# Kernel tuning notes

Hardware: AMD Instinct MI355X
Metric: run time of the kernel (lower is better)

The kernel has to match this reference:

```python
import jax, jax.numpy as jnp
import numpy as np

B, N, C = 4, 2048, 768
H, HD = 12, 64
RANK, ALPHA = 8, 16.0
SCALING = ALPHA / RANK
SCALE = HD ** -0.5


def setup_inputs() -> dict:
    key = jax.random.key(0)
    ks = jax.random.split(key, 10)
    return {
        "x": jax.random.normal(ks[0], (B, N, C), jnp.float32),
        "qkv_weight": jax.random.normal(ks[1], (3 * C, C), jnp.float32) * 0.02,
        "q_bias": jax.random.normal(ks[2], (C,), jnp.float32) * 0.02,
        "v_bias": jax.random.normal(ks[3], (C,), jnp.float32) * 0.02,
        "lora_A_qkv": jax.random.normal(ks[4], (RANK, C), jnp.float32) * 0.02,
        "lora_B_qkv": jax.random.normal(ks[5], (3 * C, RANK), jnp.float32) * 0.02,
        "proj_weight": jax.random.normal(ks[6], (C, C), jnp.float32) * 0.02,
        "proj_bias": jax.random.normal(ks[7], (C,), jnp.float32) * 0.02,
        "lora_A_proj": jax.random.normal(ks[8], (RANK, C), jnp.float32) * 0.02,
        "lora_B_proj": jax.random.normal(ks[9], (C, RANK), jnp.float32) * 0.02,
    }


def reference(x, qkv_weight, q_bias, v_bias, lora_A_qkv, lora_B_qkv,
              proj_weight, proj_bias, lora_A_proj, lora_B_proj):
    # qkv bias = [q_bias, zeros, v_bias]
    qkv_bias = jnp.concatenate([q_bias, jnp.zeros_like(v_bias), v_bias])
    qkv = jnp.einsum('bnc,oc->bno', x, qkv_weight) + qkv_bias  # [B,N,3C]
    # LoRA on qkv: (x @ A^T @ B^T) * scaling
    qkv = qkv + jnp.einsum('bnr,or->bno', jnp.einsum('bnc,rc->bnr', x, lora_A_qkv), lora_B_qkv) * SCALING
    qkv = qkv.reshape(B, N, 3, H, HD).transpose(2, 0, 3, 1, 4)  # [3,B,H,N,HD]
    q, k, v = qkv[0], qkv[1], qkv[2]
    attn = jnp.einsum('bhnd,bhmd->bhnm', q * SCALE, k)  # [B,H,N,N]
    attn = jax.nn.softmax(attn, axis=-1)
    out = jnp.einsum('bhnm,bhmd->bhnd', attn, v)
    out = out.transpose(0, 2, 1, 3).reshape(B, N, C)
    out = jnp.einsum('bnc,oc->bno', out, proj_weight) + proj_bias
    # NOTE: module applies proj LoRA to the OUTPUT of proj (faithful quirk)
    out = out + jnp.einsum('bnr,or->bno', jnp.einsum('bnc,rc->bnr', out, lora_A_proj), lora_B_proj) * SCALING
    return out
```

## Files before the change

### kernel.cpp

```cpp
#include <hip/hip_runtime.h>
#include <cstdint>
#include <cstddef>

typedef __bf16 bf16;
typedef __bf16 bf16x2_t __attribute__((ext_vector_type(2)));
typedef __bf16 bf16x4_t __attribute__((ext_vector_type(4)));
typedef __bf16 bf16x8_t __attribute__((ext_vector_type(8)));
typedef float f32x4_t __attribute__((ext_vector_type(4)));
typedef unsigned int u32;
typedef u32 u32x2_t __attribute__((ext_vector_type(2)));

#define DEV __device__ __forceinline__

static constexpr int CD  = 768;
static constexpr int C3  = 2304;
static constexpr int SEQ = 2048;
static constexpr int NB  = 4;
static constexpr int NH  = 12;
static constexpr int HDM = 64;
static constexpr int BHN = NB * NH;
static constexpr float QSCALE = 0.125f * 1.44269504088896340736f;
static constexpr float DEFER_THR = 4.0f;

DEV void async16(const void* g, void* l) {
  __builtin_amdgcn_global_load_lds(
      (const __attribute__((address_space(1))) void*)g,
      (__attribute__((address_space(3))) void*)l, 16, 0, 0);
}

DEV int swz(int r) { return (r ^ (r >> 2)) & 3; }

DEV u32 pack_bf16(float lo, float hi) {
  bf16x2_t v;
  v[0] = (bf16)lo;
  v[1] = (bf16)hi;
  return __builtin_bit_cast(u32, v);
}

DEV float max3f(float a, float b, float c) { return fmaxf(fmaxf(a, b), c); }

__global__ void k_prep_a(const float* __restrict__ x, bf16* __restrict__ xb,
                         const float* __restrict__ W, const float* __restrict__ Aq,
                         const float* __restrict__ Bq, bf16* __restrict__ We,
                         const float* __restrict__ Ap, const float* __restrict__ Wp,
                         float* __restrict__ T,
                         const float* __restrict__ bp, const float* __restrict__ Bp,
                         float* __restrict__ be) {
  __shared__ float smem[4][64];
  const int bid = blockIdx.x, tid = threadIdx.x;
  if (bid < 6912) {
    int idx = bid * 256 + tid;
    int o = idx / CD, c = idx % CD;
    float s = 0.f;
#pragma unroll
    for (int r = 0; r < 8; ++r) s += Bq[o * 8 + r] * Aq[r * CD + c];
    We[idx] = (bf16)(W[idx] + 2.0f * s);
  } else if (bid < 7008) {
    const int lb = bid - 6912;
    const int r = lb / 12, cp0 = (lb % 12) * 64;
    const int kl = tid >> 6, cpl = tid & 63;
    float s = 0.f;
    const int c0 = kl * 192;
    for (int c = c0; c < c0 + 192; ++c)
      s += Ap[r * CD + c] * Wp[(size_t)c * CD + cp0 + cpl];
    smem[kl][cpl] = s;
    __syncthreads();
    if (tid < 64)
      T[r * CD + cp0 + tid] = (smem[0][tid] + smem[1][tid]) +
                              (smem[2][tid] + smem[3][tid]);
  } else if (bid == 7008) {
    float* tl = &smem[0][0];
    const int r = tid >> 5, cl = tid & 31;
    float part = 0.f;
    for (int c = cl; c < CD; c += 32) part += Ap[r * CD + c] * bp[c];
#pragma unroll
    for (int d = 1; d < 32; d <<= 1) part += __shfl_xor(part, d);
    if (cl == 0) tl[r] = part;
    __syncthreads();
    for (int o = tid; o < CD; o += 256) {
      float s = 0.f;
#pragma unroll
      for (int rr = 0; rr < 8; ++rr) s += Bp[o * 8 + rr] * tl[rr];
      be[o] = bp[o] + 2.0f * s;
    }
  } else {
    const int n4 = (int)((size_t)NB * SEQ * CD / 4);
    int i = (bid - 7009) * 256 + tid;
    const int stride = 2048 * 256;
    for (; i < n4; i += stride) {
      float4 v = reinterpret_cast<const float4*>(x)[i];
      bf16x4_t b;
      b[0] = (bf16)v.x; b[1] = (bf16)v.y; b[2] = (bf16)v.z; b[3] = (bf16)v.w;
      reinterpret_cast<bf16x4_t*>(xb)[i] = b;
    }
  }
}

__global__ void k_prep_projw(const float* __restrict__ Wp, const float* __restrict__ Bp,
                             const float* __restrict__ T, bf16* __restrict__ We) {
  int idx = blockIdx.x * 256 + threadIdx.x;
  int o = idx / CD, cp = idx % CD;
  float s = 0.f;
#pragma unroll
  for (int r = 0; r < 8; ++r) s += Bp[o * 8 + r] * T[r * CD + cp];
  We[idx] = (bf16)(Wp[idx] + 2.0f * s);
}

__global__ __launch_bounds__(512) void k_gemm0(
    const bf16* __restrict__ Ag, const bf16* __restrict__ Bg,
    const float* __restrict__ qb, const float* __restrict__ vb,
    bf16* __restrict__ Qo, bf16* __restrict__ Ko, bf16* __restrict__ Vt) {
  __shared__ bf16 lds[2][(256 + 128) * 32];
  const int tid = threadIdx.x;
  const int w = tid >> 6, lane = tid & 63;
  const int lr = lane & 15, lg = lane >> 4;
  const int L = blockIdx.x;
  const int idx = L >> 3;
  const int m0 = ((L & 7) * 4 + idx / 18) * 256;
  const int n0 = (idx % 18) * 128;
  const int wm = w >> 1, wn = w & 1;

  const int r0 = tid >> 2, gp0 = tid & 3;
  const bf16* gA0 = Ag + (size_t)(m0 + r0) * CD + (gp0 ^ swz(r0)) * 8;
  const bf16* gA1 = Ag + (size_t)(m0 + 128 + r0) * CD + (gp0 ^ swz(r0)) * 8;
  const bf16* gB0 = Bg + (size_t)(n0 + r0) * CD + (gp0 ^ swz(r0)) * 8;

  f32x4_t acc[4][4] = {};

  auto stage = [&](int buf, int kof) {
    char* base = (char*)&lds[buf][0];
    async16(gA0 + kof, base + w * 1024);
    async16(gA1 + kof, base + 8192 + w * 1024);
    async16(gB0 + kof, base + 16384 + w * 1024);
  };

  stage(0, 0);
  int cur = 0;
  const int NK = CD / 32;
  for (int kt = 0; kt < NK; ++kt) {
    __syncthreads();
    if (kt + 1 < NK) stage(cur ^ 1, (kt + 1) * 32);
    const char* ba = (const char*)&lds[cur][0];
    const char* bb = ba + 16384;
    bf16x8_t af[4], bfr[4];
#pragma unroll
    for (int mi = 0; mi < 4; ++mi) {
      int rr = wm * 64 + mi * 16 + lr;
      af[mi] = *(const bf16x8_t*)(ba + rr * 64 + ((lg ^ swz(rr)) * 16));
    }
#pragma unroll
    for (int ni = 0; ni < 4; ++ni) {
      int rr = wn * 64 + ni * 16 + lr;
      bfr[ni] = *(const bf16x8_t*)(bb + rr * 64 + ((lg ^ swz(rr)) * 16));
    }
#pragma unroll
    for (int mi = 0; mi < 4; ++mi)
#pragma unroll
      for (int ni = 0; ni < 4; ++ni)
        acc[mi][ni] = __builtin_amdgcn_mfma_f32_16x16x32_bf16(bfr[ni], af[mi], acc[mi][ni], 0, 0, 0);
    cur ^= 1;
  }

  const int t = n0 / CD;
  if (t != 2) {
#pragma unroll
    for (int mi = 0; mi < 4; ++mi) {
      const int m = m0 + wm * 64 + mi * 16 + lr;
      const int b = m >> 11, nn = m & 2047;
#pragma unroll
      for (int ni = 0; ni < 4; ++ni) {
        const int nb = n0 + wn * 64 + ni * 16 + lg * 4;
        const int rem = nb - t * CD;
        const int h = rem >> 6, hd = rem & 63;
        const size_t oa = ((size_t)((b * NH + h) * SEQ + nn)) * HDM + hd;
        bf16x4_t o4;
        if (t == 0) {
          const float4 bias = *(const float4*)(qb + rem);
          o4[0] = (bf16)((acc[mi][ni][0] + bias.x) * QSCALE);
          o4[1] = (bf16)((acc[mi][ni][1] + bias.y) * QSCALE);
          o4[2] = (bf16)((acc[mi][ni][2] + bias.z) * QSCALE);
          o4[3] = (bf16)((acc[mi][ni][3] + bias.w) * QSCALE);
          *(bf16x4_t*)(Qo + oa) = o4;
        } else {
#pragma unroll
          for (int j = 0; j < 4; ++j) o4[j] = (bf16)acc[mi][ni][j];
          *(bf16x4_t*)(Ko + oa) = o4;
        }
      }
    }
  } else {
    bf16* tl = (bf16*)&lds[0][0];
    const int h0 = (n0 - 2 * CD) >> 6;
    const int bq = m0 >> 11;
    const int mb = m0 & 2047;
    const int r2 = tid >> 2, c2 = (tid & 3) * 32;
#pragma unroll
    for (int half = 0; half < 2; ++half) {
      __syncthreads();
      if ((wm >> 1) == half) {
#pragma unroll
        for (int mi = 0; mi < 4; ++mi) {
          const int ml = (wm & 1) * 64 + mi * 16 + lr;
#pragma unroll
          for (int ni = 0; ni < 4; ++ni) {
            const int hd = ni * 16 + lg * 4;
            const int rem = (n0 - 2 * CD) + wn * 64 + hd;
            const float4 bias = *(const float4*)(vb + rem);
            bf16* row = tl + (wn * 64 + hd) * 136 + ml;
            row[0 * 136] = (bf16)(acc[mi][ni][0] + bias.x);
            row[1 * 136] = (bf16)(acc[mi][ni][1] + bias.y);
            row[2 * 136] = (bf16)(acc[mi][ni][2] + bias.z);
            row[3 * 136] = (bf16)(acc[mi][ni][3] + bias.w);
          }
        }
      }
      __syncthreads();
      bf16* dstv = Vt + ((size_t)((bq * NH + h0 + (r2 >> 6)) * HDM) + (r2 & 63)) * SEQ
                      + mb + half * 128 + c2;
      const bf16* srcv = tl + r2 * 136 + c2;
#pragma unroll
      for (int k2 = 0; k2 < 4; ++k2)
        *(bf16x8_t*)(dstv + k2 * 8) = *(const bf16x8_t*)(srcv + k2 * 8);
    }
  }
}

__global__ __launch_bounds__(256) void k_gemm1(
    const bf16* __restrict__ Ag, const bf16* __restrict__ Bg,
    const float* __restrict__ beff, float* __restrict__ Fo) {
  __shared__ bf16 lds[2][2][128 * 32];
  const int tid = threadIdx.x;
  const int w = tid >> 6, lane = tid & 63;
  const int lr = lane & 15, lg = lane >> 4;
  const int L = blockIdx.x;
  const int idx = L >> 3;
  const int m0 = ((L & 7) * 8 + idx / 6) * 128;
  const int n0 = (idx % 6) * 128;
  const int wm = w >> 1, wn = w & 1;

  const int r0 = tid >> 2, gp0 = tid & 3;
  const int r1 = 64 + r0;
  const bf16* gA0 = Ag + (size_t)(m0 + r0) * CD + (gp0 ^ swz(r0)) * 8;
  const bf16* gA1 = Ag + (size_t)(m0 + r1) * CD + (gp0 ^ swz(r1)) * 8;
  const bf16* gB0 = Bg + (size_t)(n0 + r0) * CD + (gp0 ^ swz(r0)) * 8;
  const bf16* gB1 = Bg + (size_t)(n0 + r1) * CD + (gp0 ^ swz(r1)) * 8;
  const int dd0 = w * 1024, dd1 = 4096 + w * 1024;

  f32x4_t acc[4][4] = {};

  auto stage = [&](int buf, int kof) {
    char* ba = (char*)&lds[buf][0][0];
    char* bb = (char*)&lds[buf][1][0];
    async16(gA0 + kof, ba + dd0);
    async16(gA1 + kof, ba + dd1);
    async16(gB0 + kof, bb + dd0);
    async16(gB1 + kof, bb + dd1);
  };

  stage(0, 0);
  int cur = 0;
  const int NK = CD / 32;
  for (int kt = 0; kt < NK; ++kt) {
    __syncthreads();
    if (kt + 1 < NK) stage(cur ^ 1, (kt + 1) * 32);
    const char* ba = (const char*)&lds[cur][0][0];
    const char* bb = (const char*)&lds[cur][1][0];
    bf16x8_t af[4], bfr[4];
#pragma unroll
    for (int mi = 0; mi < 4; ++mi) {
      int rr = wm * 64 + mi * 16 + lr;
      af[mi] = *(const bf16x8_t*)(ba + rr * 64 + ((lg ^ swz(rr)) * 16));
    }
#pragma unroll
    for (int ni = 0; ni < 4; ++ni) {
      int rr = wn * 64 + ni * 16 + lr;
      bfr[ni] = *(const bf16x8_t*)(bb + rr * 64 + ((lg ^ swz(rr)) * 16));
    }
#pragma unroll
    for (int mi = 0; mi < 4; ++mi)
#pragma unroll
      for (int ni = 0; ni < 4; ++ni)
        acc[mi][ni] = __builtin_amdgcn_mfma_f32_16x16x32_bf16(bfr[ni], af[mi], acc[mi][ni], 0, 0, 0);
    cur ^= 1;
  }

#pragma unroll
  for (int mi = 0; mi < 4; ++mi) {
    const int m = m0 + wm * 64 + mi * 16 + lr;
#pragma unroll
    for (int ni = 0; ni < 4; ++ni) {
      const int nb = n0 + wn * 64 + ni * 16 + lg * 4;
      const float4 be4 = *(const float4*)(beff + nb);
      float4 o;
      o.x = acc[mi][ni][0] + be4.x;
      o.y = acc[mi][ni][1] + be4.y;
      o.z = acc[mi][ni][2] + be4.z;
      o.w = acc[mi][ni][3] + be4.w;
      *(float4*)(Fo + (size_t)m * CD + nb) = o;
    }
  }
}

__global__ __launch_bounds__(256, 3) void k_attn(const bf16* __restrict__ Q,
                                                 const bf16* __restrict__ Kg,
                                                 const bf16* __restrict__ Vt,
                                                 bf16* __restrict__ Ao) {
  __shared__ bf16 Kl[2][64 * 64];
  __shared__ bf16 Vl[2][64 * 64];
  __shared__ bf16 P[4][32 * 72];
  const int tid = threadIdx.x;
  const int w = tid >> 6, lane = tid & 63;
  const int lq = lane & 15, lg = lane >> 4;
  const int L = blockIdx.x;
  const int qb = (L >> 3) & 15;
  const int bh = (L & 7) * 6 + (L >> 7);
  const int b = bh / NH, h = bh % NH;
  const int qrow0 = qb * 128 + w * 32;

  const bf16* Qp = Q + ((size_t)bh * SEQ + qrow0) * HDM;
  const bf16* Kp = Kg + (size_t)bh * SEQ * HDM;
  const bf16* Vp = Vt + (size_t)bh * HDM * SEQ;

  const int sr = tid >> 3, scs = tid & 7;
  const int sr2 = sr + 32;
  bf16* kb0 = &Kl[0][w * 512]; bf16* kb1 = &Kl[1][w * 512];
  bf16* vb0 = &Vl[0][w * 512]; bf16* vb1 = &Vl[1][w * 512];

  auto stageKV = [&](int buf, int kb) {
    bf16* kd = buf ? kb1 : kb0;
    bf16* vd = buf ? vb1 : vb0;
    async16(Kp + (size_t)(kb + sr) * HDM + ((scs ^ (sr & 7)) * 8), kd);
    async16(Kp + (size_t)(kb + sr2) * HDM + ((scs ^ (sr2 & 7)) * 8), kd + 2048);
    async16(Vp + (size_t)sr * SEQ + kb + ((scs ^ (sr & 7)) * 8), vd);
    async16(Vp + (size_t)sr2 * SEQ + kb + ((scs ^ (sr2 & 7)) * 8), vd + 2048);
  };

  bf16x8_t qf[2][2];
#pragma unroll
  for (int qh = 0; qh < 2; ++qh)
#pragma unroll
    for (int s = 0; s < 2; ++s)
      qf[qh][s] = *(const bf16x8_t*)(Qp + (size_t)(lq + 16 * qh) * HDM + s * 32 + lg * 8);

  bf16x8_t ones;
#pragma unroll
  for (int j = 0; j < 8; ++j) ones[j] = (bf16)1.0f;

  f32x4_t oacc[2][2][4] = {};
  float mrun[2][2] = {{-1e30f, -1e30f}, {-1e30f, -1e30f}};
  float lsum[2][2] = {{0.f, 0.f}, {0.f, 0.f}};
  bf16* Pl = &P[w][0];
  const int sw = lq & 7;

  auto body = [&](const int curbuf, const int kb) {
    __syncthreads();
    if (kb + 64 < SEQ) stageKV(curbuf ^ 1, kb + 64);
    const bf16* Kc = &Kl[curbuf][0];
    const bf16* Vc = &Vl[curbuf][0];

    f32x4_t st[2][2][2];
#pragma unroll
    for (int c = 0; c < 2; ++c)
#pragma unroll
      for (int nt = 0; nt < 2; ++nt) {
        const int row = c * 32 + nt * 16 + lq;
        bf16x8_t k0 = *(const bf16x8_t*)(Kc + row * 64 + ((lg ^ sw) * 8));
        bf16x8_t k1 = *(const bf16x8_t*)(Kc + row * 64 + (((4 + lg) ^ sw) * 8));
#pragma unroll
        for (int qh = 0; qh < 2; ++qh) {
          f32x4_t z = {0.f, 0.f, 0.f, 0.f};
          z = __builtin_amdgcn_mfma_f32_16x16x32_bf16(k0, qf[qh][0], z, 0, 0, 0);
          st[c][nt][qh] = __builtin_amdgcn_mfma_f32_16x16x32_bf16(k1, qf[qh][1], z, 0, 0, 0);
        }
      }

#pragma unroll
    for (int c = 0; c < 2; ++c)
#pragma unroll
      for (int qh = 0; qh < 2; ++qh) {
        float m = max3f(st[c][0][qh][0], st[c][0][qh][1], st[c][0][qh][2]);
        float m2 = max3f(st[c][0][qh][3], st[c][1][qh][0], st[c][1][qh][1]);
        m = max3f(m, m2, st[c][1][qh][2]);
        m = fmaxf(m, st[c][1][qh][3]);
        m = fmaxf(m, __shfl_xor(m, 16));
        m = fmaxf(m, __shfl_xor(m, 32));
        if (__any(m > mrun[c][qh] + DEFER_THR)) {
          const float mnew = fmaxf(mrun[c][qh], m);
          const float corr = __builtin_amdgcn_exp2f(mrun[c][qh] - mnew);
          mrun[c][qh] = mnew;
          lsum[c][qh] *= corr;
#pragma unroll
          for (int dt = 0; dt < 4; ++dt)
#pragma unroll
            for (int j = 0; j < 4; ++j) oacc[c][qh][dt][j] *= corr;
        }
#pragma unroll
        for (int nt = 0; nt < 2; ++nt)
#pragma unroll
          for (int j = 0; j < 4; ++j)
            st[c][nt][qh][j] = __builtin_amdgcn_exp2f(st[c][nt][qh][j] - mrun[c][qh]);

#pragma unroll
        for (int nt = 0; nt < 2; ++nt) {
          u32x2_t pw = {pack_bf16(st[c][nt][qh][0], st[c][nt][qh][1]),
                        pack_bf16(st[c][nt][qh][2], st[c][nt][qh][3])};
          *(u32x2_t*)(Pl + (lq + 16 * qh) * 72 + c * 32 + nt * 16 + lg * 4) = pw;
        }
      }

#pragma unroll
    for (int c = 0; c < 2; ++c) {
      bf16x8_t pf[2];
#pragma unroll
      for (int qh = 0; qh < 2; ++qh) {
        pf[qh] = *(const bf16x8_t*)(Pl + (lq + 16 * qh) * 72 + c * 32 + lg * 8);
        const f32x4_t zz = {0.f, 0.f, 0.f, 0.f};
        f32x4_t srow = __builtin_amdgcn_mfma_f32_16x16x32_bf16(ones, pf[qh], zz, 0, 0, 0);
        lsum[c][qh] += srow[0];
      }
#pragma unroll
      for (int dt = 0; dt < 4; ++dt) {
        const int vrow = dt * 16 + lq;
        bf16x8_t vf = *(const bf16x8_t*)(Vc + vrow * 64 + (((c * 4 + lg) ^ sw) * 8));
#pragma unroll
        for (int qh = 0; qh < 2; ++qh)
          oacc[c][qh][dt] = __builtin_amdgcn_mfma_f32_16x16x32_bf16(vf, pf[qh], oacc[c][qh][dt], 0, 0, 0);
      }
    }
  };

  stageKV(0, 0);
  for (int kb = 0; kb < SEQ; kb += 128) {
    body(0, kb);
    body(1, kb + 64);
  }

#pragma unroll
  for (int qh = 0; qh < 2; ++qh) {
    const float mm = fmaxf(mrun[0][qh], mrun[1][qh]);
    const float c0 = __builtin_amdgcn_exp2f(mrun[0][qh] - mm);
    const float c1 = __builtin_amdgcn_exp2f(mrun[1][qh] - mm);
    const float inv = 1.0f / (lsum[0][qh] * c0 + lsum[1][qh] * c1);
    bf16* dst = Ao + ((size_t)b * SEQ + qrow0 + lq + 16 * qh) * CD + h * HDM;
#pragma unroll
    for (int dt = 0; dt < 4; ++dt) {
      bf16x4_t o4;
#pragma unroll
      for (int j = 0; j < 4; ++j)
        o4[j] = (bf16)((oacc[0][qh][dt][j] * c0 + oacc[1][qh][dt][j] * c1) * inv);
      *(bf16x4_t*)(dst + dt * 16 + lg * 4) = o4;
    }
  }
}

extern "C" void kernel_launch(void* const* d_in, const int* in_sizes, int n_in,
                              void* d_out, int out_size, void* d_ws, size_t ws_size,
                              hipStream_t stream) {
  const float* x    = (const float*)d_in[0];
  const float* qkvw = (const float*)d_in[1];
  const float* qb   = (const float*)d_in[2];
  const float* vb   = (const float*)d_in[3];
  const float* Aq   = (const float*)d_in[4];
  const float* Bq   = (const float*)d_in[5];
  const float* Wp   = (const float*)d_in[6];
  const float* bp   = (const float*)d_in[7];
  const float* Ap   = (const float*)d_in[8];
  const float* Bp   = (const float*)d_in[9];
  float* out = (float*)d_out;

  char* ws = (char*)d_ws;
  size_t off = 0;
  auto alloc = [&](size_t bytes) {
    void* p = ws + off;
    off += (bytes + 511) & ~size_t(511);
    return p;
  };
  const size_t M = (size_t)NB * SEQ;
  bf16* xb   = (bf16*)alloc(M * CD * 2);
  bf16* Wqe  = (bf16*)alloc((size_t)C3 * CD * 2);
  bf16* Wpe  = (bf16*)alloc((size_t)CD * CD * 2);
  float* T   = (float*)alloc(8 * CD * 4);
  float* be  = (float*)alloc(CD * 4);
  bf16* Qb   = (bf16*)alloc((size_t)BHN * SEQ * HDM * 2);
  bf16* Kb   = (bf16*)alloc((size_t)BHN * SEQ * HDM * 2);
  bf16* Vtb  = (bf16*)alloc((size_t)BHN * SEQ * HDM * 2);
  bf16* attn = xb;

  k_prep_a<<<9057, 256, 0, stream>>>(x, xb, qkvw, Aq, Bq, Wqe, Ap, Wp, T, bp, Bp, be);
  k_prep_projw<<<(CD * CD) / 256, 256, 0, stream>>>(Wp, Bp, T, Wpe);

  k_gemm0<<<576, 512, 0, stream>>>(xb, Wqe, qb, vb, Qb, Kb, Vtb);
  k_attn<<<(SEQ / 128) * BHN, 256, 0, stream>>>(Qb, Kb, Vtb, attn);
  k_gemm1<<<384, 256, 0, stream>>>(attn, Wpe, be, out);
}
```

Measured before the change: 180.7 us.

## Switch attention to 32x32x16 MFMA with register-resident P via permlane swaps

Rewrites the attention inner loop to use 32x32x16 bf16 MFMA tiles instead of 16x16x32, so each wave handles its 32 query rows as a single tile with one running max and sum. The P matrix no longer round-trips through LDS; it is repacked in registers with v_permlane32_swap to form the B operand. It also changes the LDS swizzle key and adds s_setprio around the MFMA sections. The aim is to cut LDS traffic and softmax bookkeeping per block, at the cost of larger accumulator register tiles and a dependency on a newer ISA instruction.

```diff
diff --git a/kernel.cpp b/kernel.cpp
--- a/kernel.cpp
+++ b/kernel.cpp
@@ -7,8 +7,10 @@
 typedef __bf16 bf16x4_t __attribute__((ext_vector_type(4)));
 typedef __bf16 bf16x8_t __attribute__((ext_vector_type(8)));
 typedef float f32x4_t __attribute__((ext_vector_type(4)));
+typedef float f32x16_t __attribute__((ext_vector_type(16)));
 typedef unsigned int u32;
 typedef u32 u32x2_t __attribute__((ext_vector_type(2)));
+typedef u32 u32x4_t __attribute__((ext_vector_type(4)));
 
 #define DEV __device__ __forceinline__
 
@@ -29,12 +31,16 @@
 }
 
 DEV int swz(int r) { return (r ^ (r >> 2)) & 3; }
+DEV int key8(int r) { return (r ^ (r >> 3)) & 7; }
 
 DEV u32 pack_bf16(float lo, float hi) {
   bf16x2_t v;
   v[0] = (bf16)lo;
   v[1] = (bf16)hi;
   return __builtin_bit_cast(u32, v);
+}
+DEV void pl_swap(u32& a, u32& b) {
+  asm("v_permlane32_swap_b32 %0, %1" : "+v"(a), "+v"(b));
 }
 
 DEV float max3f(float a, float b, float c) { return fmaxf(fmaxf(a, b), c); }
@@ -307,10 +313,9 @@
                                                  bf16* __restrict__ Ao) {
   __shared__ bf16 Kl[2][64 * 64];
   __shared__ bf16 Vl[2][64 * 64];
-  __shared__ bf16 P[4][32 * 72];
   const int tid = threadIdx.x;
   const int w = tid >> 6, lane = tid & 63;
-  const int lq = lane & 15, lg = lane >> 4;
+  const int ql = lane & 31, hi = lane >> 5;
   const int L = blockIdx.x;
   const int qb = (L >> 3) & 15;
   const int bh = (L & 7) * 6 + (L >> 7);
@@ -329,28 +334,24 @@
   auto stageKV = [&](int buf, int kb) {
     bf16* kd = buf ? kb1 : kb0;
     bf16* vd = buf ? vb1 : vb0;
-    async16(Kp + (size_t)(kb + sr) * HDM + ((scs ^ (sr & 7)) * 8), kd);
-    async16(Kp + (size_t)(kb + sr2) * HDM + ((scs ^ (sr2 & 7)) * 8), kd + 2048);
-    async16(Vp + (size_t)sr * SEQ + kb + ((scs ^ (sr & 7)) * 8), vd);
-    async16(Vp + (size_t)sr2 * SEQ + kb + ((scs ^ (sr2 & 7)) * 8), vd + 2048);
+    async16(Kp + (size_t)(kb + sr) * HDM + ((scs ^ key8(sr)) * 8), kd);
+    async16(Kp + (size_t)(kb + sr2) * HDM + ((scs ^ key8(sr2)) * 8), kd + 2048);
+    async16(Vp + (size_t)sr * SEQ + kb + ((scs ^ key8(sr)) * 8), vd);
+    async16(Vp + (size_t)sr2 * SEQ + kb + ((scs ^ key8(sr2)) * 8), vd + 2048);
   };
 
-  bf16x8_t qf[2][2];
-#pragma unroll
-  for (int qh = 0; qh < 2; ++qh)
-#pragma unroll
-    for (int s = 0; s < 2; ++s)
-      qf[qh][s] = *(const bf16x8_t*)(Qp + (size_t)(lq + 16 * qh) * HDM + s * 32 + lg * 8);
+  bf16x8_t qf[4];
+#pragma unroll
+  for (int s = 0; s < 4; ++s)
+    qf[s] = *(const bf16x8_t*)(Qp + (size_t)ql * HDM + s * 16 + hi * 8);
 
   bf16x8_t ones;
 #pragma unroll
   for (int j = 0; j < 8; ++j) ones[j] = (bf16)1.0f;
 
-  f32x4_t oacc[2][2][4] = {};
-  float mrun[2][2] = {{-1e30f, -1e30f}, {-1e30f, -1e30f}};
-  float lsum[2][2] = {{0.f, 0.f}, {0.f, 0.f}};
-  bf16* Pl = &P[w][0];
-  const int sw = lq & 7;
+  f32x16_t oacc[2] = {};
+  float mrun = -1e30f, lsum = 0.f;
+  const int krow = ql;
 
   auto body = [&](const int curbuf, const int kb) {
     __syncthreads();
@@ -358,75 +359,82 @@
     const bf16* Kc = &Kl[curbuf][0];
     const bf16* Vc = &Vl[curbuf][0];
 
-    f32x4_t st[2][2][2];
-#pragma unroll
-    for (int c = 0; c < 2; ++c)
-#pragma unroll
-      for (int nt = 0; nt < 2; ++nt) {
-        const int row = c * 32 + nt * 16 + lq;
-        bf16x8_t k0 = *(const bf16x8_t*)(Kc + row * 64 + ((lg ^ sw) * 8));
-        bf16x8_t k1 = *(const bf16x8_t*)(Kc + row * 64 + (((4 + lg) ^ sw) * 8));
-#pragma unroll
-        for (int qh = 0; qh < 2; ++qh) {
-          f32x4_t z = {0.f, 0.f, 0.f, 0.f};
-          z = __builtin_amdgcn_mfma_f32_16x16x32_bf16(k0, qf[qh][0], z, 0, 0, 0);
-          st[c][nt][qh] = __builtin_amdgcn_mfma_f32_16x16x32_bf16(k1, qf[qh][1], z, 0, 0, 0);
-        }
+    f32x16_t st[2];
+    __builtin_amdgcn_s_setprio(1);
+#pragma unroll
+    for (int t = 0; t < 2; ++t) {
+      const int row = t * 32 + krow;
+      const int kk = key8(row);
+      f32x16_t z = {};
+#pragma unroll
+      for (int s = 0; s < 4; ++s) {
+        bf16x8_t kf = *(const bf16x8_t*)(Kc + row * 64 + (((2 * s + hi) ^ kk) * 8));
+        z = __builtin_amdgcn_mfma_f32_32x32x16_bf16(kf, qf[s], z, 0, 0, 0);
       }
-
-#pragma unroll
-    for (int c = 0; c < 2; ++c)
-#pragma unroll
-      for (int qh = 0; qh < 2; ++qh) {
-        float m = max3f(st[c][0][qh][0], st[c][0][qh][1], st[c][0][qh][2]);
-        float m2 = max3f(st[c][0][qh][3], st[c][1][qh][0], st[c][1][qh][1]);
-        m = max3f(m, m2, st[c][1][qh][2]);
-        m = fmaxf(m, st[c][1][qh][3]);
-        m = fmaxf(m, __shfl_xor(m, 16));
-        m = fmaxf(m, __shfl_xor(m, 32));
-        if (__any(m > mrun[c][qh] + DEFER_THR)) {
-          const float mnew = fmaxf(mrun[c][qh], m);
-          const float corr = __builtin_amdgcn_exp2f(mrun[c][qh] - mnew);
-          mrun[c][qh] = mnew;
-          lsum[c][qh] *= corr;
-#pragma unroll
-          for (int dt = 0; dt < 4; ++dt)
-#pragma unroll
-            for (int j = 0; j < 4; ++j) oacc[c][qh][dt][j] *= corr;
-        }
-#pragma unroll
-        for (int nt = 0; nt < 2; ++nt)
-#pragma unroll
-          for (int j = 0; j < 4; ++j)
-            st[c][nt][qh][j] = __builtin_amdgcn_exp2f(st[c][nt][qh][j] - mrun[c][qh]);
-
-#pragma unroll
-        for (int nt = 0; nt < 2; ++nt) {
-          u32x2_t pw = {pack_bf16(st[c][nt][qh][0], st[c][nt][qh][1]),
-                        pack_bf16(st[c][nt][qh][2], st[c][nt][qh][3])};
-          *(u32x2_t*)(Pl + (lq + 16 * qh) * 72 + c * 32 + nt * 16 + lg * 4) = pw;
-        }
+      st[t] = z;
+    }
+    __builtin_amdgcn_s_setprio(0);
+
+    float m01[8];
+#pragma unroll
+    for (int i = 0; i < 8; ++i)
+      m01[i] = fmaxf(fmaxf(st[0][2 * i], st[0][2 * i + 1]),
+                     fmaxf(st[1][2 * i], st[1][2 * i + 1]));
+    float m = max3f(max3f(m01[0], m01[1], m01[2]),
+                    max3f(m01[3], m01[4], m01[5]),
+                    fmaxf(m01[6], m01[7]));
+    m = fmaxf(m, __shfl_xor(m, 32));
+    if (__any(m > mrun + DEFER_THR)) {
+      const float mnew = fmaxf(mrun, m);
+      const float corr = __builtin_amdgcn_exp2f(mrun - mnew);
+      mrun = mnew;
+      lsum *= corr;
+#pragma unroll
+      for (int dh = 0; dh < 2; ++dh)
+#pragma unroll
+        for (int r = 0; r < 16; ++r) oacc[dh][r] *= corr;
+    }
+#pragma unroll
+    for (int t = 0; t < 2; ++t)
+#pragma unroll
+      for (int r = 0; r < 16; ++r)
+        st[t][r] = __builtin_amdgcn_exp2f(st[t][r] - mrun);
+
+    bf16x8_t pf[4];
+#pragma unroll
+    for (int t = 0; t < 2; ++t) {
+      u32 c[8];
+#pragma unroll
+      for (int g = 0; g < 4; ++g) {
+        c[2 * g]     = pack_bf16(st[t][4 * g],     st[t][4 * g + 1]);
+        c[2 * g + 1] = pack_bf16(st[t][4 * g + 2], st[t][4 * g + 3]);
       }
-
-#pragma unroll
-    for (int c = 0; c < 2; ++c) {
-      bf16x8_t pf[2];
-#pragma unroll
-      for (int qh = 0; qh < 2; ++qh) {
-        pf[qh] = *(const bf16x8_t*)(Pl + (lq + 16 * qh) * 72 + c * 32 + lg * 8);
-        const f32x4_t zz = {0.f, 0.f, 0.f, 0.f};
-        f32x4_t srow = __builtin_amdgcn_mfma_f32_16x16x32_bf16(ones, pf[qh], zz, 0, 0, 0);
-        lsum[c][qh] += srow[0];
+      pl_swap(c[0], c[2]); pl_swap(c[1], c[3]);
+      pl_swap(c[4], c[6]); pl_swap(c[5], c[7]);
+      u32x4_t lo = {c[0], c[1], c[2], c[3]};
+      u32x4_t hi4 = {c[4], c[5], c[6], c[7]};
+      pf[2 * t]     = __builtin_bit_cast(bf16x8_t, lo);
+      pf[2 * t + 1] = __builtin_bit_cast(bf16x8_t, hi4);
+    }
+
+    __builtin_amdgcn_s_setprio(1);
+    f32x16_t lrow = {};
+#pragma unroll
+    for (int s = 0; s < 4; ++s)
+      lrow = __builtin_amdgcn_mfma_f32_32x32x16_bf16(ones, pf[s], lrow, 0, 0, 0);
+    lsum += lrow[0];
+
+#pragma unroll
+    for (int dh = 0; dh < 2; ++dh) {
+      const int drow = dh * 32 + ql;
+      const int kk = key8(drow);
+#pragma unroll
+      for (int s = 0; s < 4; ++s) {
+        bf16x8_t vf = *(const bf16x8_t*)(Vc + drow * 64 + (((2 * s + hi) ^ kk) * 8));
+        oacc[dh] = __builtin_amdgcn_mfma_f32_32x32x16_bf16(vf, pf[s], oacc[dh], 0, 0, 0);
       }
-#pragma unroll
-      for (int dt = 0; dt < 4; ++dt) {
-        const int vrow = dt * 16 + lq;
-        bf16x8_t vf = *(const bf16x8_t*)(Vc + vrow * 64 + (((c * 4 + lg) ^ sw) * 8));
-#pragma unroll
-        for (int qh = 0; qh < 2; ++qh)
-          oacc[c][qh][dt] = __builtin_amdgcn_mfma_f32_16x16x32_bf16(vf, pf[qh], oacc[c][qh][dt], 0, 0, 0);
-      }
-    }
+    }
+    __builtin_amdgcn_s_setprio(0);
   };
 
   stageKV(0, 0);
@@ -435,22 +443,18 @@
     body(1, kb + 64);
   }
 
-#pragma unroll
-  for (int qh = 0; qh < 2; ++qh) {
-    const float mm = fmaxf(mrun[0][qh], mrun[1][qh]);
-    const float c0 = __builtin_amdgcn_exp2f(mrun[0][qh] - mm);
-    const float c1 = __builtin_amdgcn_exp2f(mrun[1][qh] - mm);
-    const float inv = 1.0f / (lsum[0][qh] * c0 + lsum[1][qh] * c1);
-    bf16* dst = Ao + ((size_t)b * SEQ + qrow0 + lq + 16 * qh) * CD + h * HDM;
-#pragma unroll
-    for (int dt = 0; dt < 4; ++dt) {
+  const float inv = 1.0f / lsum;
+  bf16* dst = Ao + ((size_t)b * SEQ + qrow0 + ql) * CD + h * HDM;
+#pragma unroll
+  for (int dh = 0; dh < 2; ++dh)
+#pragma unroll
+    for (int g = 0; g < 4; ++g) {
+      const int d = dh * 32 + 8 * g + 4 * hi;
       bf16x4_t o4;
 #pragma unroll
-      for (int j = 0; j < 4; ++j)
-        o4[j] = (bf16)((oacc[0][qh][dt][j] * c0 + oacc[1][qh][dt][j] * c1) * inv);
-      *(bf16x4_t*)(dst + dt * 16 + lg * 4) = o4;
-    }
-  }
+      for (int j = 0; j < 4; ++j) o4[j] = (bf16)(oacc[dh][4 * g + j] * inv);
+      *(bf16x4_t*)(dst + d) = o4;
+    }
 }
 
 extern "C" void kernel_launch(void* const* d_in, const int* in_sizes, int n_in,
```

Result: no change. 177.7 us (-1.6%).
